# Kernel optimization log

Hardware: AMD Instinct MI355X
Metric: run time of the kernel (lower is better)

## Reference

```python
import jax, jax.numpy as jnp
import numpy as np

E, D, I, TOPK, N = 8, 2048, 4096, 2, 4096


def setup_inputs() -> dict:
    key = jax.random.key(0)
    k_x, k_w, k_i, k_g, k_u, k_d = jax.random.split(key, 6)
    x = jax.random.normal(k_x, (N, D), dtype=jnp.float32)
    expert_weights = jax.random.uniform(k_w, (N, TOPK), dtype=jnp.float32)
    expert_indices = jax.random.randint(k_i, (N, TOPK), 0, E).astype(jnp.int32)
    s_in = np.float32(1.0 / np.sqrt(D))
    s_mid = np.float32(1.0 / np.sqrt(I))
    # SwitchLinear weights: [num_experts, out_features, in_features]
    wg = jax.random.normal(k_g, (E, I, D), dtype=jnp.float32) * s_in
    wu = jax.random.normal(k_u, (E, I, D), dtype=jnp.float32) * s_in
    wd = jax.random.normal(k_d, (E, D, I), dtype=jnp.float32) * s_mid
    return {"x": x, "expert_weights": expert_weights,
            "expert_indices": expert_indices, "top_k": TOPK,
            "wg": wg, "wu": wu, "wd": wd}


def reference(x, expert_weights, expert_indices, top_k, wg, wu, wd):
    # out[n] = sum_k expert_weights[n,k] * Wd[e] @ (silu(Wg[e] x[n]) * (Wu[e] x[n]))
    #          with e = expert_indices[n,k].
    # Grouped-by-expert form (identical math): accumulate each expert's
    # contribution over all tokens, weighted by its routing weight (0 if not routed).
    num_experts = wg.shape[0]
    out = jnp.zeros_like(x)
    for e in range(num_experts):
        # per-token routing weight for expert e (sums over top_k slots)
        w_e = jnp.sum(jnp.where(expert_indices == e, expert_weights, 0.0), axis=-1)  # [N]
        gate = x @ wg[e].T            # [N, I]
        up = x @ wu[e].T              # [N, I]
        h = jax.nn.silu(gate) * up    # SwiGLU, [N, I]
        out = out + w_e[:, None] * (h @ wd[e].T)  # [N, D]
    return out
```

## Files before the change

### kernel.cpp

```cpp
#include <hip/hip_runtime.h>
#include <hip/hip_bf16.h>
#include <math.h>

#define E_ 8
#define D_ 2048
#define I_ 4096
#define TOPK_ 2
#define N_ 4096
#define NPAIR (N_*TOPK_)
#define PADMAX 10240
#define MAXTB256 40
#define NIB 16
#define CVTX 24
#define CH_X   (1L<<20)
#define CH_HALF (1L<<22)
#define CH_WD  (1L<<23)

typedef __attribute__((ext_vector_type(8))) short s8v;
typedef __attribute__((ext_vector_type(8))) unsigned short us8;
typedef __attribute__((ext_vector_type(4))) float f32x4;
typedef const __attribute__((address_space(1))) void* gvp;
typedef __attribute__((address_space(3))) void* lvp;

__device__ __forceinline__ unsigned short f2bf(float f) {
  union { float f; unsigned int u; } c; c.f = f;
  unsigned int u = c.u;
  u += 0x7fffu + ((u >> 16) & 1u);
  return (unsigned short)(u >> 16);
}

__device__ __forceinline__ void cvt_chunk(const float* __restrict__ src,
                                          unsigned short* __restrict__ dst,
                                          size_t off) {
  float4 a = *(const float4*)(src + off);
  float4 b = *(const float4*)(src + off + 4);
  us8 o;
  o[0]=f2bf(a.x); o[1]=f2bf(a.y); o[2]=f2bf(a.z); o[3]=f2bf(a.w);
  o[4]=f2bf(b.x); o[5]=f2bf(b.y); o[6]=f2bf(b.z); o[7]=f2bf(b.w);
  *(us8*)(dst + off) = o;
}

__device__ __forceinline__ void cvt_half(const float* __restrict__ src,
                                         unsigned short* __restrict__ dst,
                                         long chunk, int ihalf) {
  long f = chunk << 3;
  int e = (int)(f >> 22);
  long r = f & ((1L << 22) - 1);
  size_t off = ((size_t)e << 23) + ((size_t)ihalf << 22) + (size_t)r;
  cvt_chunk(src, dst, off);
}

__global__ __launch_bounds__(512)
void head_kernel(const int* __restrict__ idx, const float* __restrict__ ew,
                 int* cnt, int* offs, int* tb, int* ntb,
                 int* perm, float* wgt,
                 const float* __restrict__ x, unsigned short* __restrict__ xb,
                 const float* __restrict__ wg, unsigned short* __restrict__ wgb,
                 const float* __restrict__ wu, unsigned short* __restrict__ wub)
{
  if (blockIdx.x == 0) {
    __shared__ int scnt[E_], soff[E_ + 1], scur[E_];
    int t = threadIdx.x;
    if (t < E_) scnt[t] = 0;
    __syncthreads();
    for (int p = t; p < NPAIR; p += blockDim.x) atomicAdd(&scnt[idx[p]], 1);
    __syncthreads();
    if (t == 0) {
      int o = 0;
      for (int e = 0; e < E_; e++) {
        soff[e] = o; scur[e] = o;
        o += ((scnt[e] + 255) / 256) * 256;
      }
      soff[E_] = o;
      int T = 0;
      for (int e = 0; e < E_; e++) {
        int nb = (scnt[e] + 255) / 256;
        for (int rb = 0; rb < nb; rb++) tb[T++] = (e << 16) | rb;
      }
      *ntb = T;
      for (int e = 0; e < E_; e++) { cnt[e] = scnt[e]; offs[e] = soff[e]; }
      offs[E_] = o;
    }
    __syncthreads();
    for (int e = 0; e < E_; e++) {
      int start = soff[e] + scnt[e], end = soff[e + 1];
      for (int s = start + t; s < end; s += blockDim.x) { perm[s] = -1; wgt[s] = 0.f; }
    }
    __syncthreads();
    for (int p = t; p < NPAIR; p += blockDim.x) {
      int e = idx[p];
      int pos = atomicAdd(&scur[e], 1);
      perm[pos] = p / TOPK_;
      wgt[pos]  = ew[p];
    }
    return;
  }
  const long TOTAL = CH_X + 2 * CH_HALF;
  long c0 = (long)(blockIdx.x - 1) * 512 + threadIdx.x;
  long stride = (long)(gridDim.x - 1) * 512;
  for (long c = c0; c < TOTAL; c += stride) {
    if (c < CH_X) cvt_chunk(x, xb, (size_t)c << 3);
    else if (c < CH_X + CH_HALF) cvt_half(wg, wgb, c - CH_X, 0);
    else cvt_half(wu, wub, c - CH_X - CH_HALF, 0);
  }
}

#define A_SLAB(P,KH) (((P)*2+(KH))*8192)
#define B_SLAB(P,KH) (32768 + ((P)*2+(KH))*8192)

#define SB  __builtin_amdgcn_sched_barrier(0)
#define BARR __builtin_amdgcn_s_barrier()
#define VMW(N) asm volatile("s_waitcnt vmcnt(" #N ")" ::: "memory")
#define LGK asm volatile("s_waitcnt lgkmcnt(0)" ::: "memory")
#define PRIO1 __builtin_amdgcn_s_setprio(1)
#define PRIO0 __builtin_amdgcn_s_setprio(0)

#define LOAD_A(P,KH,MH) { \
  const unsigned short* ap_ = &smem[A_SLAB(P,KH) + aBase + (MH)*2048]; \
  af[0] = *(const s8v*)(ap_);      af[1] = *(const s8v*)(ap_+512); \
  af[2] = *(const s8v*)(ap_+1024); af[3] = *(const s8v*)(ap_+1536); }

#define LOAD_B(P,KH) { \
  const unsigned short* bp_ = &smem[B_SLAB(P,KH) + bBase]; \
  bf[0] = *(const s8v*)(bp_);      bf[1] = *(const s8v*)(bp_+512); \
  bf[2] = *(const s8v*)(bp_+1024); bf[3] = *(const s8v*)(bp_+1536); }

#define STAGE_A(T,KH,P) { \
  __builtin_amdgcn_global_load_lds((gvp)(aptr0 + (T)*64 + (KH)*32), (lvp)(&smem[A_SLAB(P,KH) + (w*2+0)*512]), 16, 0, 0); \
  __builtin_amdgcn_global_load_lds((gvp)(aptr1 + (T)*64 + (KH)*32), (lvp)(&smem[A_SLAB(P,KH) + (w*2+1)*512]), 16, 0, 0); }

#define STAGE_B(T,KH,P) { \
  __builtin_amdgcn_global_load_lds((gvp)(bptr0 + (T)*64 + (KH)*32), (lvp)(&smem[B_SLAB(P,KH) + (w*2+0)*512]), 16, 0, 0); \
  __builtin_amdgcn_global_load_lds((gvp)(bptr1 + (T)*64 + (KH)*32), (lvp)(&smem[B_SLAB(P,KH) + (w*2+1)*512]), 16, 0, 0); }

#define MFMA16(MH) { \
  _Pragma("unroll") for (int m_ = 0; m_ < 4; m_++) \
    _Pragma("unroll") for (int n_ = 0; n_ < 4; n_++) \
      acc[(MH)*4+m_][n_] = __builtin_amdgcn_mfma_f32_16x16x32_bf16(af[m_], bf[n_], acc[(MH)*4+m_][n_], 0, 0, 0); }

#define TILE_PHASES(T, P, Pn, NT_) { \
  if (T) { VMW(4); SB; } \
  LOAD_B(P, 0); LOAD_A(P, 0, 0); \
  if ((T) + 1 < (NT_)) { STAGE_A((T)+1, 1, Pn); } \
  SB; BARR; LGK; SB; \
  PRIO1; MFMA16(0); PRIO0; SB; BARR; SB; \
  LOAD_A(P, 0, 1); \
  if ((T) + 1 < (NT_)) { STAGE_B((T)+1, 1, Pn); } \
  SB; BARR; LGK; SB; \
  PRIO1; MFMA16(1); PRIO0; SB; BARR; SB; \
  if ((T) == (NT_) - 1) { VMW(0); SB; } else { VMW(4); SB; } \
  LOAD_B(P, 1); LOAD_A(P, 1, 0); \
  if ((T) + 2 < (NT_)) { STAGE_A((T)+2, 0, P); } \
  SB; BARR; LGK; SB; \
  PRIO1; MFMA16(0); PRIO0; SB; BARR; SB; \
  LOAD_A(P, 1, 1); \
  if ((T) + 2 < (NT_)) { STAGE_B((T)+2, 0, P); } \
  SB; BARR; LGK; SB; \
  PRIO1; MFMA16(1); PRIO0; SB; BARR; SB; }

#define K_LOOP(NT_) { \
  STAGE_A(0,0,0); STAGE_B(0,0,0); STAGE_A(0,1,0); STAGE_B(0,1,0); \
  STAGE_A(1,0,1); STAGE_B(1,0,1); \
  VMW(8); SB; BARR; SB; \
  _Pragma("unroll 1") \
  for (int tt = 0; tt < (NT_)/2; ++tt) { \
    TILE_PHASES(2*tt,   0, 1, NT_); \
    TILE_PHASES(2*tt+1, 1, 0, NT_); \
  } }

__global__ __launch_bounds__(512, 2)
void gu8_kernel(const unsigned short* __restrict__ xb,
                const unsigned short* __restrict__ wgb,
                const unsigned short* __restrict__ wub,
                const int* __restrict__ tb, const int* __restrict__ ntb,
                const int* __restrict__ offs, const int* __restrict__ perm,
                unsigned short* __restrict__ H,
                int i_base, int cvt_mode,
                const float* __restrict__ cs0, unsigned short* __restrict__ cd0,
                const float* __restrict__ cs1, unsigned short* __restrict__ cd1)
{
  __shared__ unsigned short smem[65536];

  if (blockIdx.x >= MAXTB256) {
    long cid = (long)(blockIdx.x - MAXTB256) + (long)CVTX * blockIdx.y;
    long c0 = cid * 512 + threadIdx.x;
    long stride = (long)CVTX * NIB * 512;
    if (cvt_mode == 1) {
      for (long c = c0; c < 2 * CH_HALF; c += stride) {
        if (c < CH_HALF) cvt_half(cs0, cd0, c, 1);
        else cvt_half(cs1, cd1, c - CH_HALF, 1);
      }
    } else {
      for (long c = c0; c < CH_WD; c += stride) cvt_chunk(cs0, cd0, (size_t)c << 3);
    }
    return;
  }

  int lid = blockIdx.y * MAXTB256 + blockIdx.x;
  int sid = (lid & 7) * (MAXTB256 * NIB / 8) + (lid >> 3);
  int bx = sid / NIB;
  int by = sid % NIB;
  if (bx >= *ntb) return;
  int ent = tb[bx];
  int e = ent >> 16, rb = ent & 0xffff;
  int slotbase = offs[e] + rb * 256;
  int i0 = i_base + by * 128;

  int tid = threadIdx.x, lane = tid & 63, w = tid >> 6;
  int wr = w >> 2, wc = w & 3;

  int cS = (lane & 7) ^ (lane >> 3);
  int rrS = 2 * (lane >> 3) + (cS >> 2);
  int kcS = (cS & 3) * 8;
  int ar0 = (w * 2 + 0) * 16 + rrS;
  int tk0 = perm[slotbase + ar0];       if (tk0 < 0) tk0 = 0;
  int tk1 = perm[slotbase + ar0 + 16];  if (tk1 < 0) tk1 = 0;
  const unsigned short* aptr0 = xb + (size_t)tk0 * D_ + kcS;
  const unsigned short* aptr1 = xb + (size_t)tk1 * D_ + kcS;
  const unsigned short* bptr0 = wgb + ((size_t)e * I_ + i0 + w * 16 + rrS) * D_ + kcS;
  const unsigned short* bptr1 = wub + ((size_t)e * I_ + i0 + w * 16 + rrS) * D_ + kcS;

  int hl = (lane & 15) >> 1;
  int pA = (((lane & 1) * 4 + (lane >> 4)) ^ hl) * 8;
  int aBase = wr * 4096 + hl * 64 + pA;
  int bBase = wc * 2048 + hl * 64 + pA;

  s8v af[4], bf[4];
  f32x4 acc[8][4];
#pragma unroll
  for (int m = 0; m < 8; m++)
#pragma unroll
    for (int n = 0; n < 4; n++) acc[m][n] = f32x4{0.f,0.f,0.f,0.f};

  K_LOOP(32);

#pragma unroll
  for (int m = 0; m < 8; m++) {
#pragma unroll
    for (int r = 0; r < 4; r++) {
      int row = wr * 128 + m * 16 + (lane >> 4) * 4 + r;
      size_t hbase = (size_t)(slotbase + row) * I_ + i0 + (lane & 15);
#pragma unroll
      for (int pr = 0; pr < 2; pr++) {
        float g = acc[m][pr*2][r];
        float u = acc[m][pr*2+1][r];
        float h = (g / (1.0f + __expf(-g))) * u;
        H[hbase + (wc * 2 + pr) * 16] = f2bf(h);
      }
    }
  }
}

__global__ __launch_bounds__(512, 2)
void down8_kernel(const unsigned short* __restrict__ H,
                  const unsigned short* __restrict__ wdb,
                  const int* __restrict__ tb, const int* __restrict__ ntb,
                  const int* __restrict__ offs, const int* __restrict__ perm,
                  const float* __restrict__ wgt,
                  float* __restrict__ out)
{
  __shared__ unsigned short smem[65536];

  int nwg = gridDim.x * gridDim.y * gridDim.z;
  int lid = (blockIdx.z * gridDim.y + blockIdx.y) * gridDim.x + blockIdx.x;
  int cpx = nwg >> 3;
  int sid = (lid & 7) * cpx + (lid >> 3);
  int bx = sid >> 4;
  int c  = sid & 15;
  int by = c & 7;
  int z  = c >> 3;
  if (bx >= *ntb) return;
  int ent = tb[bx];
  int e = ent >> 16, rb = ent & 0xffff;
  int slotbase = offs[e] + rb * 256;
  int d0 = by * 256;
  int kb = z * (I_ / 2);

  int tid = threadIdx.x, lane = tid & 63, w = tid >> 6;
  int wr = w >> 2, wc = w & 3;

  int cS = (lane & 7) ^ (lane >> 3);
  int rrS = 2 * (lane >> 3) + (cS >> 2);
  int kcS = (cS & 3) * 8;
  int ar0 = (w * 2 + 0) * 16 + rrS;
  const unsigned short* aptr0 = H + (size_t)(slotbase + ar0) * I_ + kcS + kb;
  const unsigned short* aptr1 = H + (size_t)(slotbase + ar0 + 16) * I_ + kcS + kb;
  const unsigned short* bptr0 = wdb + ((size_t)e * D_ + d0 + (w*2+0)*16 + rrS) * I_ + kcS + kb;
  const unsigned short* bptr1 = wdb + ((size_t)e * D_ + d0 + (w*2+1)*16 + rrS) * I_ + kcS + kb;

  int hl = (lane & 15) >> 1;
  int pA = (((lane & 1) * 4 + (lane >> 4)) ^ hl) * 8;
  int aBase = wr * 4096 + hl * 64 + pA;
  int bBase = wc * 2048 + hl * 64 + pA;

  s8v af[4], bf[4];
  f32x4 acc[8][4];
#pragma unroll
  for (int m = 0; m < 8; m++)
#pragma unroll
    for (int n = 0; n < 4; n++) acc[m][n] = f32x4{0.f,0.f,0.f,0.f};

  K_LOOP(32);

#pragma unroll
  for (int m = 0; m < 8; m++) {
#pragma unroll
    for (int r = 0; r < 4; r++) {
      int row = wr * 128 + m * 16 + (lane >> 4) * 4 + r;
      int s = slotbase + row;
      int tok = perm[s];
      if (tok < 0) continue;
      float wv = wgt[s];
      float* op = out + (size_t)tok * D_ + d0 + wc * 64 + (lane & 15);
#pragma unroll
      for (int n = 0; n < 4; n++)
        atomicAdd(op + n * 16, acc[m][n][r] * wv);
    }
  }
}

extern "C" void kernel_launch(void* const* d_in, const int* in_sizes, int n_in,
                              void* d_out, int out_size, void* d_ws, size_t ws_size,
                              hipStream_t stream)
{
  const float* x  = (const float*)d_in[0];
  const float* ew = (const float*)d_in[1];
  const int*  idx = (const int*)d_in[2];
  const float* wg = (const float*)d_in[4];
  const float* wu = (const float*)d_in[5];
  const float* wd = (const float*)d_in[6];
  float* out = (float*)d_out;

  char* ws = (char*)d_ws;
  int* cnt   = (int*)(ws);
  int* ntb   = (int*)(ws + 64);
  int* tb    = (int*)(ws + 128);
  int* offs  = (int*)(ws + 640);
  int* perm  = (int*)(ws + 4096);
  float* wgt = (float*)(ws + 4096 + PADMAX * 4);

  const size_t xb_off = 131072;
  const size_t xb_b   = (size_t)N_ * D_ * 2;
  const size_t H_b    = (size_t)PADMAX * I_ * 2;
  const size_t w_b    = (size_t)E_ * I_ * D_ * 2;
  unsigned short* xb  = (unsigned short*)(ws + xb_off);
  unsigned short* H   = (unsigned short*)(ws + xb_off + xb_b);
  unsigned short* wgb = (unsigned short*)(ws + xb_off + xb_b + H_b);
  unsigned short* wub = (unsigned short*)((char*)wgb + w_b);
  unsigned short* wdb = (unsigned short*)((char*)wub + w_b);

  hipMemsetAsync(d_out, 0, (size_t)N_ * D_ * sizeof(float), stream);
  head_kernel<<<2048, 512, 0, stream>>>(idx, ew, cnt, offs, tb, ntb, perm, wgt,
                                        x, xb, wg, wgb, wu, wub);
  gu8_kernel<<<dim3(MAXTB256 + CVTX, NIB), 512, 0, stream>>>(
      xb, wgb, wub, tb, ntb, offs, perm, H, 0, 1, wg, wgb, wu, wub);
  gu8_kernel<<<dim3(MAXTB256 + CVTX, NIB), 512, 0, stream>>>(
      xb, wgb, wub, tb, ntb, offs, perm, H, I_ / 2, 2, wd, wdb, (const float*)0, (unsigned short*)0);
  down8_kernel<<<dim3(MAXTB256, D_ / 256, 2), 512, 0, stream>>>(
      H, wdb, tb, ntb, offs, perm, wgt, out);
}
```

Before: 867.4 us.

## Rework MoE GEMM kernels to 1024-thread blocks with 32-wide K double-buffering

```diff
diff --git a/kernel.cpp b/kernel.cpp
--- a/kernel.cpp
+++ b/kernel.cpp
@@ -9,9 +9,8 @@
 #define N_ 4096
 #define NPAIR (N_*TOPK_)
 #define PADMAX 10240
-#define MAXTB256 40
-#define NIB 16
-#define CVTX 24
+#define MAXTB 40
+#define CVTX 12
 #define CH_X   (1L<<20)
 #define CH_HALF (1L<<22)
 #define CH_WD  (1L<<23)
@@ -105,208 +104,166 @@
   }
 }
 
-#define A_SLAB(P,KH) (((P)*2+(KH))*8192)
-#define B_SLAB(P,KH) (32768 + ((P)*2+(KH))*8192)
 
 #define SB  __builtin_amdgcn_sched_barrier(0)
 #define BARR __builtin_amdgcn_s_barrier()
 #define VMW(N) asm volatile("s_waitcnt vmcnt(" #N ")" ::: "memory")
-#define LGK asm volatile("s_waitcnt lgkmcnt(0)" ::: "memory")
 #define PRIO1 __builtin_amdgcn_s_setprio(1)
 #define PRIO0 __builtin_amdgcn_s_setprio(0)
 
-#define LOAD_A(P,KH,MH) { \
-  const unsigned short* ap_ = &smem[A_SLAB(P,KH) + aBase + (MH)*2048]; \
-  af[0] = *(const s8v*)(ap_);      af[1] = *(const s8v*)(ap_+512); \
-  af[2] = *(const s8v*)(ap_+1024); af[3] = *(const s8v*)(ap_+1536); }
-
-#define LOAD_B(P,KH) { \
-  const unsigned short* bp_ = &smem[B_SLAB(P,KH) + bBase]; \
-  bf[0] = *(const s8v*)(bp_);      bf[1] = *(const s8v*)(bp_+512); \
-  bf[2] = *(const s8v*)(bp_+1024); bf[3] = *(const s8v*)(bp_+1536); }
-
-#define STAGE_A(T,KH,P) { \
-  __builtin_amdgcn_global_load_lds((gvp)(aptr0 + (T)*64 + (KH)*32), (lvp)(&smem[A_SLAB(P,KH) + (w*2+0)*512]), 16, 0, 0); \
-  __builtin_amdgcn_global_load_lds((gvp)(aptr1 + (T)*64 + (KH)*32), (lvp)(&smem[A_SLAB(P,KH) + (w*2+1)*512]), 16, 0, 0); }
-
-#define STAGE_B(T,KH,P) { \
-  __builtin_amdgcn_global_load_lds((gvp)(bptr0 + (T)*64 + (KH)*32), (lvp)(&smem[B_SLAB(P,KH) + (w*2+0)*512]), 16, 0, 0); \
-  __builtin_amdgcn_global_load_lds((gvp)(bptr1 + (T)*64 + (KH)*32), (lvp)(&smem[B_SLAB(P,KH) + (w*2+1)*512]), 16, 0, 0); }
-
-#define MFMA16(MH) { \
-  _Pragma("unroll") for (int m_ = 0; m_ < 4; m_++) \
-    _Pragma("unroll") for (int n_ = 0; n_ < 4; n_++) \
-      acc[(MH)*4+m_][n_] = __builtin_amdgcn_mfma_f32_16x16x32_bf16(af[m_], bf[n_], acc[(MH)*4+m_][n_], 0, 0, 0); }
-
-#define TILE_PHASES(T, P, Pn, NT_) { \
-  if (T) { VMW(4); SB; } \
-  LOAD_B(P, 0); LOAD_A(P, 0, 0); \
-  if ((T) + 1 < (NT_)) { STAGE_A((T)+1, 1, Pn); } \
-  SB; BARR; LGK; SB; \
-  PRIO1; MFMA16(0); PRIO0; SB; BARR; SB; \
-  LOAD_A(P, 0, 1); \
-  if ((T) + 1 < (NT_)) { STAGE_B((T)+1, 1, Pn); } \
-  SB; BARR; LGK; SB; \
-  PRIO1; MFMA16(1); PRIO0; SB; BARR; SB; \
-  if ((T) == (NT_) - 1) { VMW(0); SB; } else { VMW(4); SB; } \
-  LOAD_B(P, 1); LOAD_A(P, 1, 0); \
-  if ((T) + 2 < (NT_)) { STAGE_A((T)+2, 0, P); } \
-  SB; BARR; LGK; SB; \
-  PRIO1; MFMA16(0); PRIO0; SB; BARR; SB; \
-  LOAD_A(P, 1, 1); \
-  if ((T) + 2 < (NT_)) { STAGE_B((T)+2, 0, P); } \
-  SB; BARR; LGK; SB; \
-  PRIO1; MFMA16(1); PRIO0; SB; BARR; SB; }
-
-#define K_LOOP(NT_) { \
-  STAGE_A(0,0,0); STAGE_B(0,0,0); STAGE_A(0,1,0); STAGE_B(0,1,0); \
-  STAGE_A(1,0,1); STAGE_B(1,0,1); \
-  VMW(8); SB; BARR; SB; \
-  _Pragma("unroll 1") \
-  for (int tt = 0; tt < (NT_)/2; ++tt) { \
-    TILE_PHASES(2*tt,   0, 1, NT_); \
-    TILE_PHASES(2*tt+1, 1, 0, NT_); \
-  } }
-
-__global__ __launch_bounds__(512, 2)
-void gu8_kernel(const unsigned short* __restrict__ xb,
-                const unsigned short* __restrict__ wgb,
-                const unsigned short* __restrict__ wub,
-                const int* __restrict__ tb, const int* __restrict__ ntb,
-                const int* __restrict__ offs, const int* __restrict__ perm,
-                unsigned short* __restrict__ H,
-                int i_base, int cvt_mode,
-                const float* __restrict__ cs0, unsigned short* __restrict__ cd0,
-                const float* __restrict__ cs1, unsigned short* __restrict__ cd1)
+#define STG(T,P) { \
+  __builtin_amdgcn_global_load_lds((gvp)(aptr + (size_t)(T)*32), (lvp)(&smem[(P)*8192 + w*512]), 16, 0, 0); \
+  __builtin_amdgcn_global_load_lds((gvp)(bptr + (size_t)(T)*32), (lvp)(&smem[16384 + (P)*8192 + w*512]), 16, 0, 0); }
+
+#define TILE32(T,P,NT_) { \
+  if ((T) == (NT_)-1) { VMW(0); } else { VMW(2); } \
+  SB; BARR; SB; \
+  { const unsigned short* ap_ = &smem[(P)*8192 + aOff]; \
+    const unsigned short* bp_ = &smem[16384 + (P)*8192 + bOff]; \
+    s8v af[4], bf[4]; \
+    af[0]=*(const s8v*)(ap_);      af[1]=*(const s8v*)(ap_+512); \
+    af[2]=*(const s8v*)(ap_+1024); af[3]=*(const s8v*)(ap_+1536); \
+    bf[0]=*(const s8v*)(bp_);      bf[1]=*(const s8v*)(bp_+512); \
+    bf[2]=*(const s8v*)(bp_+1024); bf[3]=*(const s8v*)(bp_+1536); \
+    PRIO1; \
+    _Pragma("unroll") for (int m_=0;m_<4;m_++) \
+      _Pragma("unroll") for (int n_=0;n_<4;n_++) \
+        acc[m_][n_] = __builtin_amdgcn_mfma_f32_16x16x32_bf16(af[m_], bf[n_], acc[m_][n_], 0,0,0); \
+    PRIO0; } \
+  SB; BARR; SB; \
+  if ((T)+2 < (NT_)) { STG((T)+2, P); } }
+
+#define KLOOP32(NT_) { \
+  STG(0,0); STG(1,1); \
+  _Pragma("unroll 1") for (int tt=0; tt<(NT_)/2; ++tt) { \
+    TILE32(2*tt,   0, NT_); \
+    TILE32(2*tt+1, 1, NT_); } }
+
+__global__ __launch_bounds__(1024, 4)
+void gu32_kernel(const unsigned short* __restrict__ xb,
+                 const unsigned short* __restrict__ wgb,
+                 const unsigned short* __restrict__ wub,
+                 const int* __restrict__ tb, const int* __restrict__ ntb,
+                 const int* __restrict__ offs, const int* __restrict__ perm,
+                 unsigned short* __restrict__ H,
+                 int i_base, int cvt_mode,
+                 const float* __restrict__ cs0, unsigned short* __restrict__ cd0,
+                 const float* __restrict__ cs1, unsigned short* __restrict__ cd1)
 {
-  __shared__ unsigned short smem[65536];
-
-  if (blockIdx.x >= MAXTB256) {
-    long cid = (long)(blockIdx.x - MAXTB256) + (long)CVTX * blockIdx.y;
-    long c0 = cid * 512 + threadIdx.x;
-    long stride = (long)CVTX * NIB * 512;
+  __shared__ unsigned short smem[32768];
+
+  int tid = threadIdx.x;
+  if (blockIdx.x >= MAXTB) {
+    long cid = (long)(blockIdx.x - MAXTB) + (long)CVTX * blockIdx.y;
+    long c0 = cid * 1024 + tid;
+    long stride = (long)CVTX * 16 * 1024;
     if (cvt_mode == 1) {
       for (long c = c0; c < 2 * CH_HALF; c += stride) {
         if (c < CH_HALF) cvt_half(cs0, cd0, c, 1);
         else cvt_half(cs1, cd1, c - CH_HALF, 1);
       }
-    } else {
+    } else if (cvt_mode == 2) {
       for (long c = c0; c < CH_WD; c += stride) cvt_chunk(cs0, cd0, (size_t)c << 3);
     }
     return;
   }
 
-  int lid = blockIdx.y * MAXTB256 + blockIdx.x;
-  int sid = (lid & 7) * (MAXTB256 * NIB / 8) + (lid >> 3);
-  int bx = sid / NIB;
-  int by = sid % NIB;
+  int lid = blockIdx.y * MAXTB + blockIdx.x;
+  int sid = (lid & 7) * (MAXTB * 16 / 8) + (lid >> 3);
+  int bx = sid % MAXTB;
+  int by = sid / MAXTB;
   if (bx >= *ntb) return;
   int ent = tb[bx];
   int e = ent >> 16, rb = ent & 0xffff;
   int slotbase = offs[e] + rb * 256;
   int i0 = i_base + by * 128;
 
-  int tid = threadIdx.x, lane = tid & 63, w = tid >> 6;
+  int lane = tid & 63, w = tid >> 6;
   int wr = w >> 2, wc = w & 3;
 
-  int cS = (lane & 7) ^ (lane >> 3);
-  int rrS = 2 * (lane >> 3) + (cS >> 2);
-  int kcS = (cS & 3) * 8;
-  int ar0 = (w * 2 + 0) * 16 + rrS;
-  int tk0 = perm[slotbase + ar0];       if (tk0 < 0) tk0 = 0;
-  int tk1 = perm[slotbase + ar0 + 16];  if (tk1 < 0) tk1 = 0;
-  const unsigned short* aptr0 = xb + (size_t)tk0 * D_ + kcS;
-  const unsigned short* aptr1 = xb + (size_t)tk1 * D_ + kcS;
-  const unsigned short* bptr0 = wgb + ((size_t)e * I_ + i0 + w * 16 + rrS) * D_ + kcS;
-  const unsigned short* bptr1 = wub + ((size_t)e * I_ + i0 + w * 16 + rrS) * D_ + kcS;
-
-  int hl = (lane & 15) >> 1;
-  int pA = (((lane & 1) * 4 + (lane >> 4)) ^ hl) * 8;
-  int aBase = wr * 4096 + hl * 64 + pA;
-  int bBase = wc * 2048 + hl * 64 + pA;
-
-  s8v af[4], bf[4];
-  f32x4 acc[8][4];
-#pragma unroll
-  for (int m = 0; m < 8; m++)
+  int rS = tid >> 2;
+  int cSg = (tid & 3) ^ (rS & 3);
+  int tok = perm[slotbase + rS]; if (tok < 0) tok = 0;
+  const unsigned short* aptr = xb + (size_t)tok * D_ + cSg * 8;
+  int bmat = (rS >> 4) & 1;
+  int icolS = i0 + ((rS >> 5) << 4) + (rS & 15);
+  const unsigned short* bptr = (bmat ? wub : wgb) + ((size_t)e * I_ + icolS) * D_ + cSg * 8;
+
+  int rdSw = (((lane >> 4) ^ (lane & 3)) << 3);
+  int aOff = wr * 2048 + (lane & 15) * 32 + rdSw;
+  int bOff = wc * 2048 + (lane & 15) * 32 + rdSw;
+
+  f32x4 acc[4][4];
+#pragma unroll
+  for (int m = 0; m < 4; m++)
 #pragma unroll
     for (int n = 0; n < 4; n++) acc[m][n] = f32x4{0.f,0.f,0.f,0.f};
 
-  K_LOOP(32);
-
-#pragma unroll
-  for (int m = 0; m < 8; m++) {
+  KLOOP32(64);
+
+#pragma unroll
+  for (int m = 0; m < 4; m++) {
 #pragma unroll
     for (int r = 0; r < 4; r++) {
-      int row = wr * 128 + m * 16 + (lane >> 4) * 4 + r;
+      int row = wr * 64 + m * 16 + (lane >> 4) * 4 + r;
       size_t hbase = (size_t)(slotbase + row) * I_ + i0 + (lane & 15);
 #pragma unroll
       for (int pr = 0; pr < 2; pr++) {
         float g = acc[m][pr*2][r];
         float u = acc[m][pr*2+1][r];
         float h = (g / (1.0f + __expf(-g))) * u;
-        H[hbase + (wc * 2 + pr) * 16] = f2bf(h);
+        H[hbase + (2 * wc + pr) * 16] = f2bf(h);
       }
     }
   }
 }
 
-__global__ __launch_bounds__(512, 2)
-void down8_kernel(const unsigned short* __restrict__ H,
-                  const unsigned short* __restrict__ wdb,
-                  const int* __restrict__ tb, const int* __restrict__ ntb,
-                  const int* __restrict__ offs, const int* __restrict__ perm,
-                  const float* __restrict__ wgt,
-                  float* __restrict__ out)
+__global__ __launch_bounds__(1024, 4)
+void down32_kernel(const unsigned short* __restrict__ H,
+                   const unsigned short* __restrict__ wdb,
+                   const int* __restrict__ tb, const int* __restrict__ ntb,
+                   const int* __restrict__ offs, const int* __restrict__ perm,
+                   const float* __restrict__ wgt,
+                   float* __restrict__ out)
 {
-  __shared__ unsigned short smem[65536];
-
-  int nwg = gridDim.x * gridDim.y * gridDim.z;
-  int lid = (blockIdx.z * gridDim.y + blockIdx.y) * gridDim.x + blockIdx.x;
-  int cpx = nwg >> 3;
-  int sid = (lid & 7) * cpx + (lid >> 3);
-  int bx = sid >> 4;
-  int c  = sid & 15;
-  int by = c & 7;
-  int z  = c >> 3;
+  __shared__ unsigned short smem[32768];
+
+  int tid = threadIdx.x;
+  int lid = blockIdx.y * MAXTB + blockIdx.x;
+  int sid = (lid & 7) * (MAXTB * 8 / 8) + (lid >> 3);
+  int bx = sid % MAXTB;
+  int by = sid / MAXTB;
   if (bx >= *ntb) return;
   int ent = tb[bx];
   int e = ent >> 16, rb = ent & 0xffff;
   int slotbase = offs[e] + rb * 256;
   int d0 = by * 256;
-  int kb = z * (I_ / 2);
-
-  int tid = threadIdx.x, lane = tid & 63, w = tid >> 6;
+
+  int lane = tid & 63, w = tid >> 6;
   int wr = w >> 2, wc = w & 3;
 
-  int cS = (lane & 7) ^ (lane >> 3);
-  int rrS = 2 * (lane >> 3) + (cS >> 2);
-  int kcS = (cS & 3) * 8;
-  int ar0 = (w * 2 + 0) * 16 + rrS;
-  const unsigned short* aptr0 = H + (size_t)(slotbase + ar0) * I_ + kcS + kb;
-  const unsigned short* aptr1 = H + (size_t)(slotbase + ar0 + 16) * I_ + kcS + kb;
-  const unsigned short* bptr0 = wdb + ((size_t)e * D_ + d0 + (w*2+0)*16 + rrS) * I_ + kcS + kb;
-  const unsigned short* bptr1 = wdb + ((size_t)e * D_ + d0 + (w*2+1)*16 + rrS) * I_ + kcS + kb;
-
-  int hl = (lane & 15) >> 1;
-  int pA = (((lane & 1) * 4 + (lane >> 4)) ^ hl) * 8;
-  int aBase = wr * 4096 + hl * 64 + pA;
-  int bBase = wc * 2048 + hl * 64 + pA;
-
-  s8v af[4], bf[4];
-  f32x4 acc[8][4];
-#pragma unroll
-  for (int m = 0; m < 8; m++)
+  int rS = tid >> 2;
+  int cSg = (tid & 3) ^ (rS & 3);
+  const unsigned short* aptr = H + (size_t)(slotbase + rS) * I_ + cSg * 8;
+  const unsigned short* bptr = wdb + ((size_t)e * D_ + d0 + rS) * I_ + cSg * 8;
+
+  int rdSw = (((lane >> 4) ^ (lane & 3)) << 3);
+  int aOff = wr * 2048 + (lane & 15) * 32 + rdSw;
+  int bOff = wc * 2048 + (lane & 15) * 32 + rdSw;
+
+  f32x4 acc[4][4];
+#pragma unroll
+  for (int m = 0; m < 4; m++)
 #pragma unroll
     for (int n = 0; n < 4; n++) acc[m][n] = f32x4{0.f,0.f,0.f,0.f};
 
-  K_LOOP(32);
-
-#pragma unroll
-  for (int m = 0; m < 8; m++) {
+  KLOOP32(128);
+
+#pragma unroll
+  for (int m = 0; m < 4; m++) {
 #pragma unroll
     for (int r = 0; r < 4; r++) {
-      int row = wr * 128 + m * 16 + (lane >> 4) * 4 + r;
+      int row = wr * 64 + m * 16 + (lane >> 4) * 4 + r;
       int s = slotbase + row;
       int tok = perm[s];
       if (tok < 0) continue;
@@ -352,10 +309,11 @@
   hipMemsetAsync(d_out, 0, (size_t)N_ * D_ * sizeof(float), stream);
   head_kernel<<<2048, 512, 0, stream>>>(idx, ew, cnt, offs, tb, ntb, perm, wgt,
                                         x, xb, wg, wgb, wu, wub);
-  gu8_kernel<<<dim3(MAXTB256 + CVTX, NIB), 512, 0, stream>>>(
+  gu32_kernel<<<dim3(MAXTB + CVTX, 16), 1024, 0, stream>>>(
       xb, wgb, wub, tb, ntb, offs, perm, H, 0, 1, wg, wgb, wu, wub);
-  gu8_kernel<<<dim3(MAXTB256 + CVTX, NIB), 512, 0, stream>>>(
-      xb, wgb, wub, tb, ntb, offs, perm, H, I_ / 2, 2, wd, wdb, (const float*)0, (unsigned short*)0);
-  down8_kernel<<<dim3(MAXTB256, D_ / 256, 2), 512, 0, stream>>>(
+  gu32_kernel<<<dim3(MAXTB + CVTX, 16), 1024, 0, stream>>>(
+      xb, wgb, wub, tb, ntb, offs, perm, H, I_ / 2, 2, wd, wdb,
+      (const float*)0, (unsigned short*)0);
+  down32_kernel<<<dim3(MAXTB, 8), 1024, 0, stream>>>(
       H, wdb, tb, ntb, offs, perm, wgt, out);
 }
```

Measured after the change: 829.3 us. 4.4% less time.
